# Optimization experiments

Hardware: AMD Instinct MI355X
Metric: run time of the kernel (lower is better)

Reference implementation:

```python
import jax, jax.numpy as jnp
import numpy as np

B, L, H, Q = 64, 512, 1024, 64
VA_H = 256


def setup_inputs() -> dict:
    key = jax.random.key(0)
    ks = jax.random.split(key, 10)
    hidden_states = jax.random.normal(ks[0], (B, L, H), dtype=jnp.float32)
    quad_spans = jax.random.randint(ks[1], (B, Q, 4), 0, L, dtype=jnp.int64)
    quad_mask = jnp.ones((B, Q), dtype=jnp.int32)
    s = 0.02
    W1 = jax.random.normal(ks[2], (3 * H, VA_H), dtype=jnp.float32) * s
    b1 = jnp.zeros((VA_H,), dtype=jnp.float32)
    W2 = jax.random.normal(ks[3], (VA_H, VA_H // 2), dtype=jnp.float32) * s
    b2 = jnp.zeros((VA_H // 2,), dtype=jnp.float32)
    W3 = jax.random.normal(ks[4], (VA_H // 2, 2), dtype=jnp.float32) * s
    b3 = jnp.zeros((2,), dtype=jnp.float32)
    return {"hidden_states": hidden_states, "quad_spans": quad_spans,
            "quad_mask": quad_mask, "W1": W1, "b1": b1, "W2": W2, "b2": b2,
            "W3": W3, "b3": b3}


def _pool_spans(hidden_states, quad_spans, quad_mask):
    # hidden_states [B,L,H]; quad_spans [B,Q,4]; quad_mask [B,Q]
    Bn, Ln, Hn = hidden_states.shape
    pos = jnp.arange(Ln)[None, None, :]                      # [1,1,L]
    asp_s = quad_spans[:, :, 0:1]
    asp_e = quad_spans[:, :, 1:2]
    opi_s = quad_spans[:, :, 2:3]
    opi_e = quad_spans[:, :, 3:4]
    asp_valid = asp_s >= 2
    opi_valid = opi_s >= 2
    sep = pos == 1                                           # [SEP] fallback
    asp_m = ((pos >= asp_s) & (pos <= asp_e) & asp_valid) | (~asp_valid & sep)
    opi_m = ((pos >= opi_s) & (pos <= opi_e) & opi_valid) | (~opi_valid & sep)
    qm = (quad_mask != 0)[:, :, None]
    asp_f = (asp_m & qm).astype(hidden_states.dtype)         # [B,Q,L]
    opi_f = (opi_m & qm).astype(hidden_states.dtype)
    h_asp = jnp.einsum('bql,blh->bqh', asp_f, hidden_states) / jnp.clip(
        asp_f.sum(-1, keepdims=True), 1.0, None)
    h_opi = jnp.einsum('bql,blh->bqh', opi_f, hidden_states) / jnp.clip(
        opi_f.sum(-1, keepdims=True), 1.0, None)
    return h_asp, h_opi


def reference(hidden_states, quad_spans, quad_mask, W1, b1, W2, b2, W3, b3):
    h_asp, h_opi = _pool_spans(hidden_states, quad_spans, quad_mask)
    h_pair = jnp.concatenate([h_asp, h_opi, h_asp * h_opi], axis=-1)  # [B,Q,3H]
    x = jax.nn.gelu(h_pair @ W1 + b1, approximate=False)   # torch GELU = exact
    x = jax.nn.gelu(x @ W2 + b2, approximate=False)        # dropout: eval mode
    x = x @ W3 + b3                                        # [B,Q,2]
    va = jax.nn.sigmoid(x) * 8.0 + 1.0
    return va * quad_mask[:, :, None].astype(va.dtype)
```

## Files before the change

kernel.cpp:

```cpp
#include <hip/hip_runtime.h>
#include <math.h>


typedef __attribute__((ext_vector_type(4))) float f32x4;
typedef __attribute__((ext_vector_type(8))) short bf16x8;

#define NPAIR 4096
#define LSEQ 512
#define HDIM 1024

#if defined(__has_builtin)
#if __has_builtin(__builtin_amdgcn_global_load_lds)
#define HAVE_GLDS 1
#endif
#endif
#ifndef HAVE_GLDS
#define HAVE_GLDS 0
#endif

__device__ __forceinline__ unsigned int pack2(float lo, float hi) {
  const unsigned int a = __float_as_uint(lo) + 0x8000u;
  const unsigned int b = __float_as_uint(hi) + 0x8000u;
  return __builtin_amdgcn_perm(b, a, 0x07060302u);
}
__device__ __forceinline__ unsigned short f2bf(float f) {
  return (unsigned short)((__float_as_uint(f) + 0x8000u) >> 16);
}
__device__ __forceinline__ float gelu(float x) {
  return 0.5f * x * (1.f + erff(x * 0.70710678118654752f));
}

__global__ __launch_bounds__(256, 4) void pool_mfma_kernel(
    const float* __restrict__ hs, const int* __restrict__ spans,
    const int* __restrict__ qmask, unsigned short* __restrict__ hpair) {
  __shared__ __align__(16) unsigned char smem[34816];
  __shared__ float scl[128];
  typedef unsigned short BlT[64][40];
  BlT* Bl = (BlT*)smem;
  float(*S)[68] = (float(*)[68])smem;

  const int b = blockIdx.x >> 4;
  const int n0 = (blockIdx.x & 15) * 64;
  const int tid = threadIdx.x;
  const int lane = tid & 63;
  const int lm = lane & 15, quad = lane >> 4;
  const int wm = (tid >> 6) * 32;

  const bool is64 =
      (spans[1] == 0) && (spans[3] == 0) && (spans[5] == 0) && (spans[7] == 0);

  auto span_of = [&](int r, int& s, int& e) {
    const int q = r & 63, t = r >> 6;
    const int idx = (b * 64 + q) * 4 + t * 2;
    s = is64 ? spans[idx * 2] : spans[idx];
    e = is64 ? spans[idx * 2 + 2] : spans[idx + 1];
    if (s < 2) { s = 1; e = 1; }
  };
  int s0, e0, s1, e1;
  span_of(wm + lm, s0, e0);
  span_of(wm + 16 + lm, s1, e1);

  if (tid < 128) {
    int s, e;
    span_of(tid, s, e);
    const int c = (e >= s) ? (e - s + 1) : 0;
    const float sc = 1.f / (float)(c < 1 ? 1 : c);
    scl[tid] = (qmask[b * 64 + (tid & 63)] != 0) ? sc : 0.f;
  }

  f32x4 acc[2][4];
#pragma unroll
  for (int f = 0; f < 2; ++f)
#pragma unroll
    for (int g = 0; g < 4; ++g) acc[f][g] = f32x4{0.f, 0.f, 0.f, 0.f};

  const float* hsb = hs + (size_t)b * (LSEQ * HDIM);
  const int nl = tid & 63;
  const int kw = (tid >> 6) * 8;

  auto load8 = [&](int kbase, unsigned int (&tmp)[4]) {
    const float* src = hsb + (size_t)(kbase + kw) * HDIM + n0 + nl;
#pragma unroll
    for (int i = 0; i < 4; ++i) {
      const float f0 = src[(size_t)(2 * i) * HDIM];
      const float f1 = src[(size_t)(2 * i + 1) * HDIM];
      tmp[i] = pack2(f0, f1);
    }
  };

  unsigned int tmp[4];
  load8(0, tmp);
  *(uint4*)&Bl[0][nl][kw] = make_uint4(tmp[0], tmp[1], tmp[2], tmp[3]);

  for (int it = 0; it < 16; ++it) {
    const int k0 = it * 32;
    __syncthreads();
    if (it < 15) load8(k0 + 32, tmp);

    bf16x8 a0, a1;
#pragma unroll
    for (int j = 0; j < 8; ++j) {
      const int k = k0 + quad * 8 + j;
      a0[j] = (short)((k >= s0 && k <= e0) ? 0x3F80 : 0);
      a1[j] = (short)((k >= s1 && k <= e1) ? 0x3F80 : 0);
    }
    const BlT& Bc = Bl[it & 1];
#pragma unroll
    for (int g = 0; g < 4; ++g) {
      bf16x8 bg = *(const bf16x8*)&Bc[g * 16 + lm][quad * 8];
      acc[0][g] = __builtin_amdgcn_mfma_f32_16x16x32_bf16(a0, bg, acc[0][g], 0, 0, 0);
      acc[1][g] = __builtin_amdgcn_mfma_f32_16x16x32_bf16(a1, bg, acc[1][g], 0, 0, 0);
    }
    if (it < 15) {
      *(uint4*)&Bl[(it + 1) & 1][nl][kw] = make_uint4(tmp[0], tmp[1], tmp[2], tmp[3]);
    }
  }

  __syncthreads();
#pragma unroll
  for (int f = 0; f < 2; ++f)
#pragma unroll
    for (int g = 0; g < 4; ++g)
#pragma unroll
      for (int r = 0; r < 4; ++r)
        S[wm + f * 16 + quad * 4 + r][g * 16 + lm] = acc[f][g][r];
  __syncthreads();

  const int q = tid >> 2;
  const int cg = (tid & 3) * 16;
  const float sA = scl[q], sO = scl[64 + q];
  unsigned short* dst = hpair + (size_t)(b * 64 + q) * 3072 + n0 + cg;
#pragma unroll
  for (int h = 0; h < 2; ++h) {
    float a[8], o[8];
#pragma unroll
    for (int i = 0; i < 8; ++i) {
      a[i] = S[q][cg + h * 8 + i] * sA;
      o[i] = S[64 + q][cg + h * 8 + i] * sO;
    }
    uint4 wa, wo, wp;
    wa.x = pack2(a[0], a[1]); wa.y = pack2(a[2], a[3]);
    wa.z = pack2(a[4], a[5]); wa.w = pack2(a[6], a[7]);
    wo.x = pack2(o[0], o[1]); wo.y = pack2(o[2], o[3]);
    wo.z = pack2(o[4], o[5]); wo.w = pack2(o[6], o[7]);
    wp.x = pack2(a[0] * o[0], a[1] * o[1]); wp.y = pack2(a[2] * o[2], a[3] * o[3]);
    wp.z = pack2(a[4] * o[4], a[5] * o[5]); wp.w = pack2(a[6] * o[6], a[7] * o[7]);
    *(uint4*)(dst + h * 8) = wa;
    *(uint4*)(dst + 1024 + h * 8) = wo;
    *(uint4*)(dst + 2048 + h * 8) = wp;
  }
}

__global__ void transpose_w1(const float* __restrict__ W1,
                             unsigned short* __restrict__ W1T) {
  __shared__ float t[32][33];
  const int R = 3072, C = 256;
  const int c0 = (blockIdx.x & 7) * 32, r0 = (blockIdx.x >> 3) * 32;
  const int x = threadIdx.x, y = threadIdx.y;
#pragma unroll
  for (int i = 0; i < 32; i += 8)
    t[y + i][x] = W1[(size_t)(r0 + y + i) * C + c0 + x];
  __syncthreads();
#pragma unroll
  for (int i = 0; i < 32; i += 8)
    W1T[(size_t)(c0 + y + i) * R + r0 + x] = f2bf(t[x][y + i]);
}

__global__ __launch_bounds__(256) void gemm_bt_partial(
    const unsigned short* __restrict__ A, const unsigned short* __restrict__ Bt,
    float* __restrict__ P, int M, int N, int K, int KH) {
  __shared__ __align__(16) unsigned short Al[64][32];
  __shared__ __align__(16) unsigned short Bl[64][32];
  const int bm = blockIdx.x * 64, bn = blockIdx.y * 64;
  const int kz = blockIdx.z * KH;
  const int tid = threadIdx.x;
  const int wave = tid >> 6, lane = tid & 63;
  const int wm = (wave & 1) * 32, wn = (wave >> 1) * 32;
  const int lm = lane & 15, lk = (lane >> 4) * 8;

  const int srow = wave * 16 + (lane >> 2);
  const int scol = (lane & 3) * 8;
  const unsigned short* ga = A + (size_t)(bm + srow) * K + kz + scol;
  const unsigned short* gb = Bt + (size_t)(bn + srow) * K + kz + scol;
  unsigned short* la = &Al[0][0] + wave * 512;
  unsigned short* lb = &Bl[0][0] + wave * 512;

  f32x4 acc00 = {0.f, 0.f, 0.f, 0.f}, acc01 = {0.f, 0.f, 0.f, 0.f};
  f32x4 acc10 = {0.f, 0.f, 0.f, 0.f}, acc11 = {0.f, 0.f, 0.f, 0.f};

  for (int k0 = 0; k0 < KH; k0 += 32) {
#if HAVE_GLDS
    __builtin_amdgcn_global_load_lds(ga + k0, la, 16, 0, 0);
    __builtin_amdgcn_global_load_lds(gb + k0, lb, 16, 0, 0);
#else
    *(uint4*)(la + lane * 8) = *(const uint4*)(ga + k0);
    *(uint4*)(lb + lane * 8) = *(const uint4*)(gb + k0);
#endif
    __syncthreads();
    bf16x8 a0 = *(const bf16x8*)&Al[wm + lm][lk];
    bf16x8 a1 = *(const bf16x8*)&Al[wm + 16 + lm][lk];
    bf16x8 b0 = *(const bf16x8*)&Bl[wn + lm][lk];
    bf16x8 b1 = *(const bf16x8*)&Bl[wn + 16 + lm][lk];
    acc00 = __builtin_amdgcn_mfma_f32_16x16x32_bf16(a0, b0, acc00, 0, 0, 0);
    acc01 = __builtin_amdgcn_mfma_f32_16x16x32_bf16(a0, b1, acc01, 0, 0, 0);
    acc10 = __builtin_amdgcn_mfma_f32_16x16x32_bf16(a1, b0, acc10, 0, 0, 0);
    acc11 = __builtin_amdgcn_mfma_f32_16x16x32_bf16(a1, b1, acc11, 0, 0, 0);
    __syncthreads();
  }

  float* Pz = P + (size_t)blockIdx.z * M * N;
  const int r0 = bm + wm + ((lane >> 4) << 2);
  const int c0 = bn + wn + lm;
  auto emit = [&](f32x4 v, int row0, int col) {
#pragma unroll
    for (int r = 0; r < 4; ++r) Pz[(size_t)(row0 + r) * N + col] = v[r];
  };
  emit(acc00, r0, c0);
  emit(acc10, r0 + 16, c0);
  emit(acc01, r0, c0 + 16);
  emit(acc11, r0 + 16, c0 + 16);
}

__global__ __launch_bounds__(256) void tail_kernel(
    const float* __restrict__ P, const float* __restrict__ b1,
    const float* __restrict__ W2, const float* __restrict__ b2,
    const float* __restrict__ W3, const float* __restrict__ b3,
    const int* __restrict__ qmask, float* __restrict__ out) {
  __shared__ __align__(16) unsigned short Bl[128 * 264];
  __shared__ __align__(16) unsigned short Al[16 * 264];
  __shared__ float S2[16][132];
  __shared__ float w3[256];

  const int m0 = blockIdx.x * 16;
  const int tid = threadIdx.x;
  const int wave = tid >> 6, lane = tid & 63;
  const int lm = lane & 15, quad = lane >> 4;
  const int wn = wave * 32;

  w3[tid] = W3[tid];

  for (int e = tid; e < 128 * 128; e += 256) {
    const int k2 = e >> 7;
    const int n = e & 127;
    const float lo = W2[(size_t)(2 * k2) * 128 + n];
    const float hi = W2[(size_t)(2 * k2 + 1) * 128 + n];
    *(unsigned int*)((char*)Bl + (size_t)n * 528 + k2 * 4) = pack2(lo, hi);
  }

  {
    const int row = tid >> 4;
    const int slot = tid & 15;
#pragma unroll
    for (int ss = 0; ss < 2; ++ss) {
      const int s = slot + ss * 16;
      const float* p0 = P + (size_t)(m0 + row) * 256 + s * 8;
      const float* p1 = p0 + (size_t)NPAIR * 256;
      float4 a0 = *(const float4*)p0, a1 = *(const float4*)(p0 + 4);
      float4 c0 = *(const float4*)p1, c1 = *(const float4*)(p1 + 4);
      float4 ba = *(const float4*)(b1 + s * 8);
      float4 bb = *(const float4*)(b1 + s * 8 + 4);
      const float v0 = gelu(a0.x + c0.x + ba.x);
      const float v1 = gelu(a0.y + c0.y + ba.y);
      const float v2 = gelu(a0.z + c0.z + ba.z);
      const float v3 = gelu(a0.w + c0.w + ba.w);
      const float v4 = gelu(a1.x + c1.x + bb.x);
      const float v5 = gelu(a1.y + c1.y + bb.y);
      const float v6 = gelu(a1.z + c1.z + bb.z);
      const float v7 = gelu(a1.w + c1.w + bb.w);
      uint4 w;
      w.x = pack2(v0, v1); w.y = pack2(v2, v3);
      w.z = pack2(v4, v5); w.w = pack2(v6, v7);
      *(uint4*)((char*)Al + (size_t)row * 528 + s * 16) = w;
    }
  }
  __syncthreads();

  f32x4 acc[2];
  acc[0] = f32x4{0.f, 0.f, 0.f, 0.f};
  acc[1] = f32x4{0.f, 0.f, 0.f, 0.f};
#pragma unroll
  for (int ks = 0; ks < 8; ++ks) {
    bf16x8 a = *(const bf16x8*)((char*)Al + (size_t)lm * 528 + ks * 64 + quad * 16);
#pragma unroll
    for (int g = 0; g < 2; ++g) {
      const int n = wn + g * 16 + lm;
      bf16x8 b = *(const bf16x8*)((char*)Bl + (size_t)n * 528 + ks * 64 + quad * 16);
      acc[g] = __builtin_amdgcn_mfma_f32_16x16x32_bf16(a, b, acc[g], 0, 0, 0);
    }
  }

#pragma unroll
  for (int g = 0; g < 2; ++g) {
    const int col = wn + g * 16 + lm;
    const float bc = b2[col];
#pragma unroll
    for (int r = 0; r < 4; ++r) S2[quad * 4 + r][col] = gelu(acc[g][r] + bc);
  }
  __syncthreads();

  if (tid < 128) {
    const int row = tid >> 3, o = (tid >> 2) & 1, q4 = tid & 3;
    float part = 0.f;
#pragma unroll 8
    for (int c = q4; c < 128; c += 4) part += S2[row][c] * w3[c * 2 + o];
    part += __shfl_xor(part, 1);
    part += __shfl_xor(part, 2);
    if (q4 == 0) {
      const int pair = m0 + row;
      const float a = part + b3[o];
      const float qmf = (float)qmask[pair];
      out[pair * 2 + o] = ((1.f / (1.f + expf(-a))) * 8.f + 1.f) * qmf;
    }
  }
}

extern "C" void kernel_launch(void* const* d_in, const int* in_sizes, int n_in,
                              void* d_out, int out_size, void* d_ws,
                              size_t ws_size, hipStream_t stream) {
  const float* hs = (const float*)d_in[0];
  const int* spans = (const int*)d_in[1];
  const int* qmask = (const int*)d_in[2];
  const float* W1 = (const float*)d_in[3];
  const float* b1 = (const float*)d_in[4];
  const float* W2 = (const float*)d_in[5];
  const float* b2 = (const float*)d_in[6];
  const float* W3 = (const float*)d_in[7];
  const float* b3 = (const float*)d_in[8];
  float* out = (float*)d_out;

  const size_t HPAIR_B = 25165824;
  const size_t P_B = 8388608;

  char* ws = (char*)d_ws;
  size_t off = 0;
  unsigned short* hpair = (unsigned short*)(ws + off); off += HPAIR_B;
  float* P = (float*)(ws + off);                       off += P_B;
  unsigned short* W1T = (unsigned short*)(ws + off);

  transpose_w1<<<768, dim3(32, 8), 0, stream>>>(W1, W1T);
  pool_mfma_kernel<<<1024, 256, 0, stream>>>(hs, spans, qmask, hpair);
  gemm_bt_partial<<<dim3(64, 4, 2), 256, 0, stream>>>(hpair, W1T, P, NPAIR,
                                                      256, 3072, 1536);
  tail_kernel<<<256, 256, 0, stream>>>(P, b1, W2, b2, W3, b3, qmask, out);
}
```

Baseline: 267.6 us.

## Retile W1 GEMM to double-buffered 128x128 with split-K 4; pretranspose W2

```diff
diff --git a/kernel.cpp b/kernel.cpp
--- a/kernel.cpp
+++ b/kernel.cpp
@@ -151,82 +151,110 @@
   }
 }
 
-__global__ void transpose_w1(const float* __restrict__ W1,
-                             unsigned short* __restrict__ W1T) {
+__global__ void transpose_two(const float* __restrict__ W1,
+                              unsigned short* __restrict__ W1T,
+                              const float* __restrict__ W2,
+                              unsigned short* __restrict__ W2T) {
   __shared__ float t[32][33];
-  const int R = 3072, C = 256;
-  const int c0 = (blockIdx.x & 7) * 32, r0 = (blockIdx.x >> 3) * 32;
+  const float* in;
+  unsigned short* out;
+  int R, C, c0, r0;
+  int blk = blockIdx.x;
+  if (blk < 768) {
+    in = W1; out = W1T; R = 3072; C = 256;
+    c0 = (blk & 7) * 32; r0 = (blk >> 3) * 32;
+  } else {
+    blk -= 768;
+    in = W2; out = W2T; R = 256; C = 128;
+    c0 = (blk & 3) * 32; r0 = (blk >> 2) * 32;
+  }
   const int x = threadIdx.x, y = threadIdx.y;
 #pragma unroll
   for (int i = 0; i < 32; i += 8)
-    t[y + i][x] = W1[(size_t)(r0 + y + i) * C + c0 + x];
+    t[y + i][x] = in[(size_t)(r0 + y + i) * C + c0 + x];
   __syncthreads();
 #pragma unroll
   for (int i = 0; i < 32; i += 8)
-    W1T[(size_t)(c0 + y + i) * R + r0 + x] = f2bf(t[x][y + i]);
-}
-
-__global__ __launch_bounds__(256) void gemm_bt_partial(
+    out[(size_t)(c0 + y + i) * R + r0 + x] = f2bf(t[x][y + i]);
+}
+
+__global__ __launch_bounds__(256) void gemm_bt_128(
     const unsigned short* __restrict__ A, const unsigned short* __restrict__ Bt,
     float* __restrict__ P, int M, int N, int K, int KH) {
-  __shared__ __align__(16) unsigned short Al[64][32];
-  __shared__ __align__(16) unsigned short Bl[64][32];
-  const int bm = blockIdx.x * 64, bn = blockIdx.y * 64;
+  __shared__ __align__(16) unsigned short Al[2][128][32];
+  __shared__ __align__(16) unsigned short Bl[2][128][32];
+  const int bm = blockIdx.x * 128, bn = blockIdx.y * 128;
   const int kz = blockIdx.z * KH;
   const int tid = threadIdx.x;
   const int wave = tid >> 6, lane = tid & 63;
-  const int wm = (wave & 1) * 32, wn = (wave >> 1) * 32;
+  const int wm = (wave & 1) * 64, wn = (wave >> 1) * 64;
   const int lm = lane & 15, lk = (lane >> 4) * 8;
 
-  const int srow = wave * 16 + (lane >> 2);
+  const int srow = wave * 32 + (lane >> 2);
   const int scol = (lane & 3) * 8;
   const unsigned short* ga = A + (size_t)(bm + srow) * K + kz + scol;
   const unsigned short* gb = Bt + (size_t)(bn + srow) * K + kz + scol;
-  unsigned short* la = &Al[0][0] + wave * 512;
-  unsigned short* lb = &Bl[0][0] + wave * 512;
-
-  f32x4 acc00 = {0.f, 0.f, 0.f, 0.f}, acc01 = {0.f, 0.f, 0.f, 0.f};
-  f32x4 acc10 = {0.f, 0.f, 0.f, 0.f}, acc11 = {0.f, 0.f, 0.f, 0.f};
-
-  for (int k0 = 0; k0 < KH; k0 += 32) {
+  unsigned short* laA[2] = {&Al[0][wave * 32][0], &Al[1][wave * 32][0]};
+  unsigned short* laB[2] = {&Bl[0][wave * 32][0], &Bl[1][wave * 32][0]};
+
+  f32x4 acc[4][4];
+#pragma unroll
+  for (int i = 0; i < 4; ++i)
+#pragma unroll
+    for (int j = 0; j < 4; ++j) acc[i][j] = f32x4{0.f, 0.f, 0.f, 0.f};
+
+  auto stage = [&](int u, int k0) {
 #if HAVE_GLDS
-    __builtin_amdgcn_global_load_lds(ga + k0, la, 16, 0, 0);
-    __builtin_amdgcn_global_load_lds(gb + k0, lb, 16, 0, 0);
+    __builtin_amdgcn_global_load_lds(ga + k0, laA[u], 16, 0, 0);
+    __builtin_amdgcn_global_load_lds(ga + (size_t)16 * K + k0, laA[u] + 16 * 32, 16, 0, 0);
+    __builtin_amdgcn_global_load_lds(gb + k0, laB[u], 16, 0, 0);
+    __builtin_amdgcn_global_load_lds(gb + (size_t)16 * K + k0, laB[u] + 16 * 32, 16, 0, 0);
 #else
-    *(uint4*)(la + lane * 8) = *(const uint4*)(ga + k0);
-    *(uint4*)(lb + lane * 8) = *(const uint4*)(gb + k0);
+    *(uint4*)(laA[u] + lane * 8) = *(const uint4*)(ga + k0);
+    *(uint4*)(laA[u] + 16 * 32 + lane * 8) = *(const uint4*)(ga + (size_t)16 * K + k0);
+    *(uint4*)(laB[u] + lane * 8) = *(const uint4*)(gb + k0);
+    *(uint4*)(laB[u] + 16 * 32 + lane * 8) = *(const uint4*)(gb + (size_t)16 * K + k0);
 #endif
+  };
+
+  const int NT = KH / 32;
+  stage(0, 0);
+  for (int t = 0; t < NT; ++t) {
     __syncthreads();
-    bf16x8 a0 = *(const bf16x8*)&Al[wm + lm][lk];
-    bf16x8 a1 = *(const bf16x8*)&Al[wm + 16 + lm][lk];
-    bf16x8 b0 = *(const bf16x8*)&Bl[wn + lm][lk];
-    bf16x8 b1 = *(const bf16x8*)&Bl[wn + 16 + lm][lk];
-    acc00 = __builtin_amdgcn_mfma_f32_16x16x32_bf16(a0, b0, acc00, 0, 0, 0);
-    acc01 = __builtin_amdgcn_mfma_f32_16x16x32_bf16(a0, b1, acc01, 0, 0, 0);
-    acc10 = __builtin_amdgcn_mfma_f32_16x16x32_bf16(a1, b0, acc10, 0, 0, 0);
-    acc11 = __builtin_amdgcn_mfma_f32_16x16x32_bf16(a1, b1, acc11, 0, 0, 0);
-    __syncthreads();
+    if (t + 1 < NT) stage((t + 1) & 1, (t + 1) * 32);
+    const int u = t & 1;
+    bf16x8 af[4], bf[4];
+#pragma unroll
+    for (int i = 0; i < 4; ++i) {
+      af[i] = *(const bf16x8*)&Al[u][wm + i * 16 + lm][lk];
+      bf[i] = *(const bf16x8*)&Bl[u][wn + i * 16 + lm][lk];
+    }
+#pragma unroll
+    for (int i = 0; i < 4; ++i)
+#pragma unroll
+      for (int j = 0; j < 4; ++j)
+        acc[i][j] = __builtin_amdgcn_mfma_f32_16x16x32_bf16(af[i], bf[j], acc[i][j], 0, 0, 0);
   }
 
   float* Pz = P + (size_t)blockIdx.z * M * N;
-  const int r0 = bm + wm + ((lane >> 4) << 2);
-  const int c0 = bn + wn + lm;
-  auto emit = [&](f32x4 v, int row0, int col) {
-#pragma unroll
-    for (int r = 0; r < 4; ++r) Pz[(size_t)(row0 + r) * N + col] = v[r];
-  };
-  emit(acc00, r0, c0);
-  emit(acc10, r0 + 16, c0);
-  emit(acc01, r0, c0 + 16);
-  emit(acc11, r0 + 16, c0 + 16);
+  const int rq = (lane >> 4) << 2;
+#pragma unroll
+  for (int i = 0; i < 4; ++i)
+#pragma unroll
+    for (int j = 0; j < 4; ++j) {
+      const int r0 = bm + wm + i * 16 + rq;
+      const int c0 = bn + wn + j * 16 + lm;
+#pragma unroll
+      for (int r = 0; r < 4; ++r)
+        Pz[(size_t)(r0 + r) * N + c0] = acc[i][j][r];
+    }
 }
 
 __global__ __launch_bounds__(256) void tail_kernel(
     const float* __restrict__ P, const float* __restrict__ b1,
-    const float* __restrict__ W2, const float* __restrict__ b2,
+    const unsigned short* __restrict__ W2T, const float* __restrict__ b2,
     const float* __restrict__ W3, const float* __restrict__ b3,
     const int* __restrict__ qmask, float* __restrict__ out) {
-  __shared__ __align__(16) unsigned short Bl[128 * 264];
   __shared__ __align__(16) unsigned short Al[16 * 264];
   __shared__ float S2[16][132];
   __shared__ float w3[256];
@@ -239,37 +267,33 @@
 
   w3[tid] = W3[tid];
 
-  for (int e = tid; e < 128 * 128; e += 256) {
-    const int k2 = e >> 7;
-    const int n = e & 127;
-    const float lo = W2[(size_t)(2 * k2) * 128 + n];
-    const float hi = W2[(size_t)(2 * k2 + 1) * 128 + n];
-    *(unsigned int*)((char*)Bl + (size_t)n * 528 + k2 * 4) = pack2(lo, hi);
-  }
-
   {
     const int row = tid >> 4;
     const int slot = tid & 15;
 #pragma unroll
     for (int ss = 0; ss < 2; ++ss) {
       const int s = slot + ss * 16;
-      const float* p0 = P + (size_t)(m0 + row) * 256 + s * 8;
-      const float* p1 = p0 + (size_t)NPAIR * 256;
-      float4 a0 = *(const float4*)p0, a1 = *(const float4*)(p0 + 4);
-      float4 c0 = *(const float4*)p1, c1 = *(const float4*)(p1 + 4);
-      float4 ba = *(const float4*)(b1 + s * 8);
-      float4 bb = *(const float4*)(b1 + s * 8 + 4);
-      const float v0 = gelu(a0.x + c0.x + ba.x);
-      const float v1 = gelu(a0.y + c0.y + ba.y);
-      const float v2 = gelu(a0.z + c0.z + ba.z);
-      const float v3 = gelu(a0.w + c0.w + ba.w);
-      const float v4 = gelu(a1.x + c1.x + bb.x);
-      const float v5 = gelu(a1.y + c1.y + bb.y);
-      const float v6 = gelu(a1.z + c1.z + bb.z);
-      const float v7 = gelu(a1.w + c1.w + bb.w);
+      const float* pb = P + (size_t)(m0 + row) * 256 + s * 8;
+      float v[8];
+      {
+        float4 ba = *(const float4*)(b1 + s * 8);
+        float4 bb = *(const float4*)(b1 + s * 8 + 4);
+        v[0] = ba.x; v[1] = ba.y; v[2] = ba.z; v[3] = ba.w;
+        v[4] = bb.x; v[5] = bb.y; v[6] = bb.z; v[7] = bb.w;
+      }
+#pragma unroll
+      for (int z = 0; z < 4; ++z) {
+        const float* pz = pb + (size_t)z * ((size_t)NPAIR * 256);
+        float4 a0 = *(const float4*)pz;
+        float4 a1 = *(const float4*)(pz + 4);
+        v[0] += a0.x; v[1] += a0.y; v[2] += a0.z; v[3] += a0.w;
+        v[4] += a1.x; v[5] += a1.y; v[6] += a1.z; v[7] += a1.w;
+      }
       uint4 w;
-      w.x = pack2(v0, v1); w.y = pack2(v2, v3);
-      w.z = pack2(v4, v5); w.w = pack2(v6, v7);
+      w.x = pack2(gelu(v[0]), gelu(v[1]));
+      w.y = pack2(gelu(v[2]), gelu(v[3]));
+      w.z = pack2(gelu(v[4]), gelu(v[5]));
+      w.w = pack2(gelu(v[6]), gelu(v[7]));
       *(uint4*)((char*)Al + (size_t)row * 528 + s * 16) = w;
     }
   }
@@ -284,7 +308,7 @@
 #pragma unroll
     for (int g = 0; g < 2; ++g) {
       const int n = wn + g * 16 + lm;
-      bf16x8 b = *(const bf16x8*)((char*)Bl + (size_t)n * 528 + ks * 64 + quad * 16);
+      bf16x8 b = *(const bf16x8*)(W2T + (size_t)n * 256 + ks * 32 + quad * 8);
       acc[g] = __builtin_amdgcn_mfma_f32_16x16x32_bf16(a, b, acc[g], 0, 0, 0);
     }
   }
@@ -329,17 +353,19 @@
   float* out = (float*)d_out;
 
   const size_t HPAIR_B = 25165824;
-  const size_t P_B = 8388608;
+  const size_t P_B = 16777216;
+  const size_t W1T_B = 1572864;
 
   char* ws = (char*)d_ws;
   size_t off = 0;
   unsigned short* hpair = (unsigned short*)(ws + off); off += HPAIR_B;
   float* P = (float*)(ws + off);                       off += P_B;
-  unsigned short* W1T = (unsigned short*)(ws + off);
-
-  transpose_w1<<<768, dim3(32, 8), 0, stream>>>(W1, W1T);
+  unsigned short* W1T = (unsigned short*)(ws + off);   off += W1T_B;
+  unsigned short* W2T = (unsigned short*)(ws + off);
+
+  transpose_two<<<800, dim3(32, 8), 0, stream>>>(W1, W1T, W2, W2T);
   pool_mfma_kernel<<<1024, 256, 0, stream>>>(hs, spans, qmask, hpair);
-  gemm_bt_partial<<<dim3(64, 4, 2), 256, 0, stream>>>(hpair, W1T, P, NPAIR,
-                                                      256, 3072, 1536);
-  tail_kernel<<<256, 256, 0, stream>>>(P, b1, W2, b2, W3, b3, qmask, out);
-}
+  gemm_bt_128<<<dim3(32, 2, 4), 256, 0, stream>>>(hpair, W1T, P, NPAIR,
+                                                  256, 3072, 768);
+  tail_kernel<<<256, 256, 0, stream>>>(P, b1, W2T, b2, W3, b3, qmask, out);
+}
```

After: 237.2 us. -11.4%, faster.
